# Kernel optimization log

Measured on AMD Instinct MI355X. Metric: run time of the kernel, lower is better.

Reference implementation:

```python
import jax, jax.numpy as jnp
import numpy as np

N, E, IN_DIM, H, D = 100000, 1600000, 128, 4, 32


def setup_inputs() -> dict:
    key = jax.random.key(0)
    ks = jax.random.split(key, 8)
    glorot = lambda k, shape: jax.random.uniform(
        k, shape, jnp.float32, -1.0, 1.0) * np.sqrt(6.0 / (shape[0] + shape[1]))
    return {
        "x": jax.random.normal(ks[0], (N, IN_DIM), jnp.float32),
        "row": jax.random.randint(ks[1], (E,), 0, N, jnp.int32),
        "col": jax.random.randint(ks[2], (E,), 0, N, jnp.int32),
        "W_l": glorot(ks[3], (IN_DIM, H * D)),
        "W_r": glorot(ks[4], (IN_DIM, H * D)),
        "a1w": glorot(ks[5], (IN_DIM, H)),
        "a2w": glorot(ks[6], (IN_DIM, H)),
        "bias": jnp.zeros((H * D,), jnp.float32),
    }


def reference(x, row, col, W_l, W_r, a1w, a2w, bias):
    n = x.shape[0]  # num_nodes (= graph[0].max()+1 with dense random rows)
    x_l = (x @ W_l).reshape(n, H, D)          # [N,H,D]
    x_r = x @ W_r                              # [N,H*D]
    # per-edge attention logits: a1[row] + a2[col], leaky-relu(0.2)
    attn = jax.nn.leaky_relu((x @ a1w)[row] + (x @ a2w)[col], 0.2)  # [E,H]
    # segment softmax over destination rows (numerically stable)
    m = jax.ops.segment_max(attn, row, num_segments=n)               # [N,H]
    e = jnp.exp(attn - m[row])
    s = jax.ops.segment_sum(e, row, num_segments=n)                  # [N,H]
    attn_d = e / s[row]                                              # [E,H]
    # per-head SpMM: scatter-add weighted source features to destinations
    msgs = attn_d[:, :, None] * x_l[col]                             # [E,H,D]
    out = jax.ops.segment_sum(msgs, row, num_segments=n).reshape(n, H * D)
    return out + x_r + bias
```

## Files before the change

kernel.cpp:

```cpp
#include <hip/hip_runtime.h>


typedef short bfvec8 __attribute__((ext_vector_type(8)));
typedef float f32x4  __attribute__((ext_vector_type(4)));

#define BK 256
#define CAP 6144
#define EPB 4096
#define REC 256

__device__ __forceinline__ unsigned short f2bf(float f) {
  union { float f; unsigned int i; } v; v.f = f;
  unsigned int r = v.i + 0x7fffu + ((v.i >> 16) & 1u);
  return (unsigned short)(r >> 16);
}

__global__ __launch_bounds__(128) void wprep_k(
    const float* __restrict__ Wl, const float* __restrict__ Wr,
    const float* __restrict__ a1w, const float* __restrict__ a2w,
    unsigned short* __restrict__ Wtg)
{
  const int n = blockIdx.x;
  const int y = blockIdx.y;
  const int k = threadIdx.x;
  const float* W = y ? Wr : Wl;
  const float* A = y ? a2w : a1w;
  const float LOG2E = 1.4426950408889634f;
  float v = (n < 128) ? W[(size_t)k * 128 + n] : A[k * 4 + (n - 128)] * LOG2E;
  Wtg[((size_t)y * 132 + n) * 128 + k] = f2bf(v);
}

__global__ __launch_bounds__(256) void gemm_mfma(
    const float* __restrict__ x, const unsigned short* __restrict__ Wtg,
    const float* __restrict__ bias,
    char* __restrict__ xls, float* __restrict__ out,
    float* __restrict__ s1, float* __restrict__ s2, int N)
{
  __shared__ unsigned short xs[64][136];
  __shared__ unsigned short Ws[132][136];
  const int t = threadIdx.x;
  const int n0 = blockIdx.x * 64;

  for (int i = t; i < 2048; i += 256) {
    int rr = i >> 5, kc = (i & 31) << 2;
    float4 v = make_float4(0.f, 0.f, 0.f, 0.f);
    int n = n0 + rr;
    if (n < N) v = *(const float4*)&x[(size_t)n * 128 + kc];
    unsigned int lo = (unsigned int)f2bf(v.x) | ((unsigned int)f2bf(v.y) << 16);
    unsigned int hi = (unsigned int)f2bf(v.z) | ((unsigned int)f2bf(v.w) << 16);
    *(uint2*)&xs[rr][kc] = make_uint2(lo, hi);
  }

  const int w    = t >> 6;
  const int lane = t & 63;
  const int m    = lane & 15;
  const int quad = lane >> 4;

  #pragma unroll
  for (int y = 0; y < 2; ++y) {
    const unsigned short* Wt = Wtg + (size_t)y * 132 * 128;
    if (y) __syncthreads();
    for (int i = t; i < 2112; i += 256) {
      int nr = i >> 4, kc = (i & 15) << 3;
      *(uint4*)&Ws[nr][kc] = *(const uint4*)&Wt[(size_t)nr * 128 + kc];
    }
    __syncthreads();

    f32x4 acc[9];
    #pragma unroll
    for (int i = 0; i < 9; ++i) acc[i] = (f32x4){0.f, 0.f, 0.f, 0.f};

    #pragma unroll
    for (int kc = 0; kc < 128; kc += 32) {
      bfvec8 af = *(const bfvec8*)&xs[16 * w + m][kc + quad * 8];
      #pragma unroll
      for (int nt = 0; nt < 9; ++nt) {
        int nr = nt * 16 + m; if (nr > 131) nr = 131;
        bfvec8 bfr = *(const bfvec8*)&Ws[nr][kc + quad * 8];
        acc[nt] = __builtin_amdgcn_mfma_f32_16x16x32_bf16(af, bfr, acc[nt], 0, 0, 0);
      }
    }

    #pragma unroll
    for (int nt = 0; nt < 8; ++nt) {
      int c = nt * 16 + m;
      float b = y ? bias[c] : 0.f;
      #pragma unroll
      for (int r = 0; r < 4; ++r) {
        int n = n0 + 16 * w + quad * 4 + r;
        if (n < N) {
          float v = acc[nt][r] + b;
          if (y) out[(size_t)n * 128 + c] = v;
          else   *(unsigned short*)(xls + ((size_t)n << 8) + 2 * c) = f2bf(v);
        }
      }
    }
    if (m < 4) {
      #pragma unroll
      for (int r = 0; r < 4; ++r) {
        int n = n0 + 16 * w + quad * 4 + r;
        if (n < N) {
          if (y) s2[n * 4 + m] = acc[8][r];
          else   s1[n * 4 + m] = acc[8][r];
        }
      }
    }
  }
}

__global__ __launch_bounds__(512) void init_k(int* __restrict__ bcur, int NBK) {
  int b = threadIdx.x;
  if (b < NBK) bcur[b] = b * CAP;
}

__global__ __launch_bounds__(256) void bin_k(const int* __restrict__ row,
    const int* __restrict__ col, int* __restrict__ bcur,
    unsigned int* __restrict__ binned, int E, int NBK)
{
  __shared__ int h[512];
  __shared__ int base[512];
  const int t = threadIdx.x;
  const int e0 = blockIdx.x * EPB;
  const int e1 = min(e0 + EPB, E);

  int rloc[16];
  for (int i = t; i < NBK; i += 256) h[i] = 0;
  __syncthreads();
  #pragma unroll
  for (int k = 0; k < 16; ++k) {
    int e = e0 + t + (k << 8);
    rloc[k] = (e < e1) ? row[e] : -1;
    if (rloc[k] >= 0) atomicAdd(&h[rloc[k] >> 8], 1);
  }
  __syncthreads();
  for (int i = t; i < NBK; i += 256) {
    int c = h[i];
    base[i] = c ? atomicAdd(&bcur[i], c) : 0;
  }
  __syncthreads();
  for (int i = t; i < NBK; i += 256) h[i] = 0;
  __syncthreads();
  #pragma unroll
  for (int k = 0; k < 16; ++k) {
    int e = e0 + t + (k << 8);
    if (e < e1) {
      int r = rloc[k];
      unsigned c = (unsigned)col[e];
      int b = r >> 8;
      int rk = atomicAdd(&h[b], 1);
      binned[base[b] + rk] = ((unsigned)(r & 255) << 17) | c;
    }
  }
}

__global__ __launch_bounds__(256) void csr_k(const unsigned int* __restrict__ binned,
    const int* __restrict__ bcur, int* __restrict__ offs, int* __restrict__ deg,
    unsigned int* __restrict__ colsort, int N)
{
  __shared__ int h[BK];
  __shared__ int sh[BK];
  const int t = threadIdx.x;
  const int b = blockIdx.x;
  const int lo = b * BK;
  const int e0 = b * CAP;
  const int e1 = bcur[b];

  h[t] = 0;
  __syncthreads();
  for (int i = e0 + t; i < e1; i += 256)
    atomicAdd(&h[binned[i] >> 17], 1);
  __syncthreads();

  int v = h[t];
  sh[t] = v;
  __syncthreads();
  for (int off = 1; off < 256; off <<= 1) {
    int tv = (t >= off) ? sh[t - off] : 0;
    __syncthreads();
    sh[t] += tv;
    __syncthreads();
  }
  int ex = sh[t] - v;
  int node = lo + t;
  if (node < N) { offs[node] = e0 + ex; deg[node] = v; }

  h[t] = ex;
  __syncthreads();
  for (int i = e0 + t; i < e1; i += 256) {
    unsigned p = binned[i];
    int rlo = p >> 17;
    unsigned c = p & 0x1FFFFu;
    int pos = atomicAdd(&h[rlo], 1);
    colsort[e0 + pos] = c << 8;
  }
}

__global__ __launch_bounds__(256) void agg_k(const int* __restrict__ offs,
    const int* __restrict__ deg, const unsigned int* __restrict__ colsort,
    const float* __restrict__ s1, const float* __restrict__ s2,
    const char* __restrict__ xls, float* __restrict__ out, int N)
{
  const int lane = threadIdx.x & 63;
  const int n = blockIdx.x * 4 + (threadIdx.x >> 6);
  if (n >= N) return;
  const int e0 = offs[n], e1 = e0 + deg[n];
  const int h  = lane >> 4;
  const int hp = lane & 3;
  const int jj = (lane >> 2) & 7;
  const float s1c = s1[n * 4 + hp];
  const unsigned lane4 = (unsigned)(lane << 2);
  const unsigned hp4   = (unsigned)(hp << 2);
  const char* s2b = (const char*)s2;

  float acc0 = 0.f, acc1 = 0.f, wsum = 0.f;
  int i0 = e0;
  for (; i0 + 8 <= e1; i0 += 8) {
    unsigned csl = colsort[i0 + jj];
    float z2 = *(const float*)(s2b + ((csl >> 4) + hp4));
    float z = s1c + z2;
    z = fmaxf(z, 0.2f * z);
    float wv = exp2f(z);

    unsigned cs[8];
    #pragma unroll
    for (int j = 0; j < 8; ++j) cs[j] = colsort[i0 + j];
    unsigned pv[8];
    #pragma unroll
    for (int j = 0; j < 8; ++j)
      pv[j] = *(const unsigned*)(xls + (cs[j] + lane4));

    #pragma unroll
    for (int j = 0; j < 8; ++j) {
      float wj = __shfl(wv, (j << 2) | h);
      wsum += wj;
      union { unsigned u; float f; } lo, hi;
      lo.u = pv[j] << 16;
      hi.u = pv[j] & 0xffff0000u;
      acc0 += wj * lo.f;
      acc1 += wj * hi.f;
    }
  }
  if (i0 < e1) {
    const int rem = e1 - i0;
    unsigned csl = colsort[i0 + (jj < rem ? jj : rem - 1)];
    float z2 = *(const float*)(s2b + ((csl >> 4) + hp4));
    float z = s1c + z2;
    z = fmaxf(z, 0.2f * z);
    float wv = (jj < rem) ? exp2f(z) : 0.f;

    unsigned cs[8];
    #pragma unroll
    for (int j = 0; j < 8; ++j) cs[j] = colsort[i0 + (j < rem ? j : rem - 1)];
    unsigned pv[8];
    #pragma unroll
    for (int j = 0; j < 8; ++j)
      pv[j] = *(const unsigned*)(xls + (cs[j] + lane4));

    #pragma unroll
    for (int j = 0; j < 8; ++j) {
      float wj = __shfl(wv, (j << 2) | h);
      wsum += wj;
      union { unsigned u; float f; } lo, hi;
      lo.u = pv[j] << 16;
      hi.u = pv[j] & 0xffff0000u;
      acc0 += wj * lo.f;
      acc1 += wj * hi.f;
    }
  }

  float inv = (wsum > 0.f) ? (1.0f / wsum) : 0.f;
  const size_t o = (size_t)n * 128 + 2 * lane;
  float2 xr = *(const float2*)&out[o];
  float2 res; res.x = acc0 * inv + xr.x; res.y = acc1 * inv + xr.y;
  *(float2*)&out[o] = res;
}

extern "C" void kernel_launch(void* const* d_in, const int* in_sizes, int n_in,
                              void* d_out, int out_size, void* d_ws, size_t ws_size,
                              hipStream_t stream) {
  const float* x    = (const float*)d_in[0];
  const int*   row  = (const int*)d_in[1];
  const int*   col  = (const int*)d_in[2];
  const float* Wl   = (const float*)d_in[3];
  const float* Wr   = (const float*)d_in[4];
  const float* a1w  = (const float*)d_in[5];
  const float* a2w  = (const float*)d_in[6];
  const float* bias = (const float*)d_in[7];
  float* out = (float*)d_out;
  const int N = in_sizes[0] / 128;
  const int E = in_sizes[1];
  (void)n_in; (void)out_size; (void)ws_size;

  const int NBK = (N + BK - 1) / BK;

  char* ws = (char*)d_ws;
  size_t off = 0;
  auto carve = [&](size_t bytes) { void* p = ws + off; off += (bytes + 255) & ~(size_t)255; return p; };
  char* xls            = (char*)carve((size_t)N * REC);
  float* s1            = (float*)carve((size_t)N * 4 * 4);
  float* s2            = (float*)carve((size_t)N * 4 * 4);
  int* offs            = (int*)carve((size_t)N * 4);
  int* deg             = (int*)carve((size_t)N * 4);
  unsigned int* colsort= (unsigned int*)carve((size_t)NBK * CAP * 4);
  unsigned int* binned = (unsigned int*)carve((size_t)NBK * CAP * 4);
  int* bcur            = (int*)carve((size_t)NBK * 4);
  unsigned short* Wtg  = (unsigned short*)carve((size_t)2 * 132 * 128 * 2);

  wprep_k  <<<dim3(132, 2), 128, 0, stream>>>(Wl, Wr, a1w, a2w, Wtg);
  gemm_mfma<<<(N + 63) / 64, 256, 0, stream>>>(x, Wtg, bias, xls, out, s1, s2, N);
  init_k   <<<1, 512, 0, stream>>>(bcur, NBK);
  bin_k    <<<(E + EPB - 1) / EPB, 256, 0, stream>>>(row, col, bcur, binned, E, NBK);
  csr_k    <<<NBK, 256, 0, stream>>>(binned, bcur, offs, deg, colsort, N);
  agg_k    <<<(N + 3) / 4, 256, 0, stream>>>(offs, deg, colsort, s1, s2, xls, out, N);
}
```

Baseline: 285.4 us.

## Merge attention projections into one MFMA tile, pad atomics, add nontemporal accesses

The two attention projections (a1w and a2w) are packed into a single 8-column B fragment computed only in the first GEMM pass and held in registers. This removes the ninth MFMA column tile from the second pass and shrinks the shared W tile. Bucket cursors are padded to separate cache lines to reduce atomic contention. Many global loads and stores across the GEMM, binning, CSR and aggregation kernels are switched to nontemporal variants to limit cache pollution from streaming data. Nontemporal hints could hurt data that is reused later, such as colsort and xls in L2.

```diff
diff --git a/kernel.cpp b/kernel.cpp
--- a/kernel.cpp
+++ b/kernel.cpp
@@ -3,11 +3,13 @@
 
 typedef short bfvec8 __attribute__((ext_vector_type(8)));
 typedef float f32x4  __attribute__((ext_vector_type(4)));
+typedef float f32x2  __attribute__((ext_vector_type(2)));
 
 #define BK 256
 #define CAP 6144
 #define EPB 4096
 #define REC 256
+#define BSTR 16
 
 __device__ __forceinline__ unsigned short f2bf(float f) {
   union { float f; unsigned int i; } v; v.f = f;
@@ -24,10 +26,13 @@
   const int y = blockIdx.y;
   const int k = threadIdx.x;
   const float* W = y ? Wr : Wl;
-  const float* A = y ? a2w : a1w;
   const float LOG2E = 1.4426950408889634f;
-  float v = (n < 128) ? W[(size_t)k * 128 + n] : A[k * 4 + (n - 128)] * LOG2E;
-  Wtg[((size_t)y * 132 + n) * 128 + k] = f2bf(v);
+  float v;
+  if (n < 128)      v = W[(size_t)k * 128 + n];
+  else if (y)       v = 0.f;
+  else if (n < 132) v = a1w[k * 4 + (n - 128)] * LOG2E;
+  else              v = a2w[k * 4 + (n - 132)] * LOG2E;
+  Wtg[((size_t)y * 136 + n) * 128 + k] = f2bf(v);
 }
 
 __global__ __launch_bounds__(256) void gemm_mfma(
@@ -37,17 +42,17 @@
     float* __restrict__ s1, float* __restrict__ s2, int N)
 {
   __shared__ unsigned short xs[64][136];
-  __shared__ unsigned short Ws[132][136];
+  __shared__ unsigned short Ws[128][136];
   const int t = threadIdx.x;
   const int n0 = blockIdx.x * 64;
 
   for (int i = t; i < 2048; i += 256) {
     int rr = i >> 5, kc = (i & 31) << 2;
-    float4 v = make_float4(0.f, 0.f, 0.f, 0.f);
+    f32x4 v = (f32x4){0.f, 0.f, 0.f, 0.f};
     int n = n0 + rr;
-    if (n < N) v = *(const float4*)&x[(size_t)n * 128 + kc];
-    unsigned int lo = (unsigned int)f2bf(v.x) | ((unsigned int)f2bf(v.y) << 16);
-    unsigned int hi = (unsigned int)f2bf(v.z) | ((unsigned int)f2bf(v.w) << 16);
+    if (n < N) v = __builtin_nontemporal_load((const f32x4*)&x[(size_t)n * 128 + kc]);
+    unsigned int lo = (unsigned int)f2bf(v[0]) | ((unsigned int)f2bf(v[1]) << 16);
+    unsigned int hi = (unsigned int)f2bf(v[2]) | ((unsigned int)f2bf(v[3]) << 16);
     *(uint2*)&xs[rr][kc] = make_uint2(lo, hi);
   }
 
@@ -56,11 +61,19 @@
   const int m    = lane & 15;
   const int quad = lane >> 4;
 
+  bfvec8 afr[4];
+  {
+    int arow = 128 + (m < 8 ? m : 7);
+    #pragma unroll
+    for (int kc4 = 0; kc4 < 4; ++kc4)
+      afr[kc4] = *(const bfvec8*)&Wtg[(size_t)arow * 128 + kc4 * 32 + quad * 8];
+  }
+
   #pragma unroll
   for (int y = 0; y < 2; ++y) {
-    const unsigned short* Wt = Wtg + (size_t)y * 132 * 128;
+    const unsigned short* Wt = Wtg + (size_t)y * 136 * 128;
     if (y) __syncthreads();
-    for (int i = t; i < 2112; i += 256) {
+    for (int i = t; i < 2048; i += 256) {
       int nr = i >> 4, kc = (i & 15) << 3;
       *(uint4*)&Ws[nr][kc] = *(const uint4*)&Wt[(size_t)nr * 128 + kc];
     }
@@ -71,14 +84,16 @@
     for (int i = 0; i < 9; ++i) acc[i] = (f32x4){0.f, 0.f, 0.f, 0.f};
 
     #pragma unroll
-    for (int kc = 0; kc < 128; kc += 32) {
+    for (int kc4 = 0; kc4 < 4; ++kc4) {
+      const int kc = kc4 * 32;
       bfvec8 af = *(const bfvec8*)&xs[16 * w + m][kc + quad * 8];
       #pragma unroll
-      for (int nt = 0; nt < 9; ++nt) {
-        int nr = nt * 16 + m; if (nr > 131) nr = 131;
-        bfvec8 bfr = *(const bfvec8*)&Ws[nr][kc + quad * 8];
+      for (int nt = 0; nt < 8; ++nt) {
+        bfvec8 bfr = *(const bfvec8*)&Ws[nt * 16 + m][kc + quad * 8];
         acc[nt] = __builtin_amdgcn_mfma_f32_16x16x32_bf16(af, bfr, acc[nt], 0, 0, 0);
       }
+      if (y == 0)
+        acc[8] = __builtin_amdgcn_mfma_f32_16x16x32_bf16(af, afr[kc4], acc[8], 0, 0, 0);
     }
 
     #pragma unroll
@@ -90,18 +105,19 @@
         int n = n0 + 16 * w + quad * 4 + r;
         if (n < N) {
           float v = acc[nt][r] + b;
-          if (y) out[(size_t)n * 128 + c] = v;
-          else   *(unsigned short*)(xls + ((size_t)n << 8) + 2 * c) = f2bf(v);
+          if (y) __builtin_nontemporal_store(v, &out[(size_t)n * 128 + c]);
+          else   __builtin_nontemporal_store(f2bf(v),
+                     (unsigned short*)(xls + ((size_t)n << 8) + 2 * c));
         }
       }
     }
-    if (m < 4) {
+    if (y == 0 && m < 8) {
       #pragma unroll
       for (int r = 0; r < 4; ++r) {
         int n = n0 + 16 * w + quad * 4 + r;
         if (n < N) {
-          if (y) s2[n * 4 + m] = acc[8][r];
-          else   s1[n * 4 + m] = acc[8][r];
+          if (m < 4) s1[n * 4 + m] = acc[8][r];
+          else       s2[n * 4 + (m - 4)] = acc[8][r];
         }
       }
     }
@@ -110,7 +126,7 @@
 
 __global__ __launch_bounds__(512) void init_k(int* __restrict__ bcur, int NBK) {
   int b = threadIdx.x;
-  if (b < NBK) bcur[b] = b * CAP;
+  if (b < NBK) bcur[b * BSTR] = b * CAP;
 }
 
 __global__ __launch_bounds__(256) void bin_k(const int* __restrict__ row,
@@ -129,13 +145,13 @@
   #pragma unroll
   for (int k = 0; k < 16; ++k) {
     int e = e0 + t + (k << 8);
-    rloc[k] = (e < e1) ? row[e] : -1;
+    rloc[k] = (e < e1) ? __builtin_nontemporal_load(&row[e]) : -1;
     if (rloc[k] >= 0) atomicAdd(&h[rloc[k] >> 8], 1);
   }
   __syncthreads();
   for (int i = t; i < NBK; i += 256) {
     int c = h[i];
-    base[i] = c ? atomicAdd(&bcur[i], c) : 0;
+    base[i] = c ? atomicAdd(&bcur[i * BSTR], c) : 0;
   }
   __syncthreads();
   for (int i = t; i < NBK; i += 256) h[i] = 0;
@@ -145,10 +161,11 @@
     int e = e0 + t + (k << 8);
     if (e < e1) {
       int r = rloc[k];
-      unsigned c = (unsigned)col[e];
+      unsigned c = (unsigned)__builtin_nontemporal_load(&col[e]);
       int b = r >> 8;
       int rk = atomicAdd(&h[b], 1);
-      binned[base[b] + rk] = ((unsigned)(r & 255) << 17) | c;
+      __builtin_nontemporal_store(((unsigned)(r & 255) << 17) | c,
+                                  &binned[base[b] + rk]);
     }
   }
 }
@@ -163,7 +180,7 @@
   const int b = blockIdx.x;
   const int lo = b * BK;
   const int e0 = b * CAP;
-  const int e1 = bcur[b];
+  const int e1 = bcur[b * BSTR];
 
   h[t] = 0;
   __syncthreads();
@@ -191,7 +208,7 @@
     int rlo = p >> 17;
     unsigned c = p & 0x1FFFFu;
     int pos = atomicAdd(&h[rlo], 1);
-    colsort[e0 + pos] = c << 8;
+    __builtin_nontemporal_store(c << 8, &colsort[e0 + pos]);
   }
 }
 
@@ -215,7 +232,7 @@
   float acc0 = 0.f, acc1 = 0.f, wsum = 0.f;
   int i0 = e0;
   for (; i0 + 8 <= e1; i0 += 8) {
-    unsigned csl = colsort[i0 + jj];
+    unsigned csl = __builtin_nontemporal_load(&colsort[i0 + jj]);
     float z2 = *(const float*)(s2b + ((csl >> 4) + hp4));
     float z = s1c + z2;
     z = fmaxf(z, 0.2f * z);
@@ -223,7 +240,8 @@
 
     unsigned cs[8];
     #pragma unroll
-    for (int j = 0; j < 8; ++j) cs[j] = colsort[i0 + j];
+    for (int j = 0; j < 8; ++j)
+      cs[j] = __builtin_nontemporal_load(&colsort[i0 + j]);
     unsigned pv[8];
     #pragma unroll
     for (int j = 0; j < 8; ++j)
@@ -242,7 +260,7 @@
   }
   if (i0 < e1) {
     const int rem = e1 - i0;
-    unsigned csl = colsort[i0 + (jj < rem ? jj : rem - 1)];
+    unsigned csl = __builtin_nontemporal_load(&colsort[i0 + (jj < rem ? jj : rem - 1)]);
     float z2 = *(const float*)(s2b + ((csl >> 4) + hp4));
     float z = s1c + z2;
     z = fmaxf(z, 0.2f * z);
@@ -250,7 +268,8 @@
 
     unsigned cs[8];
     #pragma unroll
-    for (int j = 0; j < 8; ++j) cs[j] = colsort[i0 + (j < rem ? j : rem - 1)];
+    for (int j = 0; j < 8; ++j)
+      cs[j] = __builtin_nontemporal_load(&colsort[i0 + (j < rem ? j : rem - 1)]);
     unsigned pv[8];
     #pragma unroll
     for (int j = 0; j < 8; ++j)
@@ -269,10 +288,10 @@
   }
 
   float inv = (wsum > 0.f) ? (1.0f / wsum) : 0.f;
-  const size_t o = (size_t)n * 128 + 2 * lane;
-  float2 xr = *(const float2*)&out[o];
-  float2 res; res.x = acc0 * inv + xr.x; res.y = acc1 * inv + xr.y;
-  *(float2*)&out[o] = res;
+  f32x2* op = (f32x2*)&out[(size_t)n * 128 + 2 * lane];
+  f32x2 xr = __builtin_nontemporal_load(op);
+  f32x2 res; res[0] = acc0 * inv + xr[0]; res[1] = acc1 * inv + xr[1];
+  __builtin_nontemporal_store(res, op);
 }
 
 extern "C" void kernel_launch(void* const* d_in, const int* in_sizes, int n_in,
@@ -303,10 +322,10 @@
   int* deg             = (int*)carve((size_t)N * 4);
   unsigned int* colsort= (unsigned int*)carve((size_t)NBK * CAP * 4);
   unsigned int* binned = (unsigned int*)carve((size_t)NBK * CAP * 4);
-  int* bcur            = (int*)carve((size_t)NBK * 4);
-  unsigned short* Wtg  = (unsigned short*)carve((size_t)2 * 132 * 128 * 2);
-
-  wprep_k  <<<dim3(132, 2), 128, 0, stream>>>(Wl, Wr, a1w, a2w, Wtg);
+  int* bcur            = (int*)carve((size_t)NBK * BSTR * 4);
+  unsigned short* Wtg  = (unsigned short*)carve((size_t)2 * 136 * 128 * 2);
+
+  wprep_k  <<<dim3(136, 2), 128, 0, stream>>>(Wl, Wr, a1w, a2w, Wtg);
   gemm_mfma<<<(N + 63) / 64, 256, 0, stream>>>(x, Wtg, bias, xls, out, s1, s2, N);
   init_k   <<<1, 512, 0, stream>>>(bcur, NBK);
   bin_k    <<<(E + EPB - 1) / EPB, 256, 0, stream>>>(row, col, bcur, binned, E, NBK);
```

Measured after the change: 341.6 us. 1.2x slower.
